# Kernel tuning notes

Hardware: AMD Instinct MI355X
Metric: run time of the kernel (lower is better)

Reference implementation:

```python
import jax, jax.numpy as jnp
import numpy as np
import math

HIDDEN = 2048
N_HEADS = 32
N_KV_HEADS = 8
HEAD_DIM = HIDDEN // N_HEADS
KV_REPEATS = N_HEADS // N_KV_HEADS
INTER = 4 * HIDDEN
EPS = 1e-5
B, Q, K = 2, 2048, 2048


def setup_inputs() -> dict:
    key = jax.random.key(0)
    ks = jax.random.split(key, 10)
    s = 0.02
    return {
        "hidden_states": jax.random.normal(ks[0], (B, Q, HIDDEN), jnp.float32),
        "key_states": jax.random.normal(ks[1], (B, K, N_KV_HEADS, HEAD_DIM), jnp.float32),
        "value_states": jax.random.normal(ks[2], (B, K, N_KV_HEADS, HEAD_DIM), jnp.float32),
        "gmu_memory": jnp.zeros((1,), jnp.float32),
        "w_ln1": jnp.ones((HIDDEN,), jnp.float32),
        "w_ln2": jnp.ones((HIDDEN,), jnp.float32),
        "w_q": jax.random.normal(ks[3], (N_HEADS * HEAD_DIM, HIDDEN), jnp.float32) * s,
        "w_o": jax.random.normal(ks[4], (HIDDEN, N_HEADS * HEAD_DIM), jnp.float32) * s,
        "w_gate": jax.random.normal(ks[5], (INTER, HIDDEN), jnp.float32) * s,
        "w_up": jax.random.normal(ks[6], (INTER, HIDDEN), jnp.float32) * s,
        "w_down": jax.random.normal(ks[7], (HIDDEN, INTER), jnp.float32) * s,
        "cu_seqlens_q": jnp.array([0, 1024, 2048], jnp.int32),
        "cu_seqlens_k": jnp.array([0, 1024, 2048], jnp.int32),
    }


def _rms_norm(x, w, eps=EPS):
    var = jnp.mean(jnp.square(x), axis=-1, keepdims=True)
    return (x * jax.lax.rsqrt(var + eps)) * w


def _segment_ids(cu, length):
    # position p belongs to segment i iff cu[i] <= p < cu[i+1]
    return jnp.searchsorted(cu[1:], jnp.arange(length), side="right")


def _attn_mask(q_len, k_len, cu_q, cu_k, causal=True, window_size=None):
    seg_q = _segment_ids(cu_q, q_len)  # [Q]
    seg_k = _segment_ids(cu_k, k_len)  # [K]
    mask = seg_q[:, None] == seg_k[None, :]
    if causal:
        q_pos = jnp.arange(q_len)[:, None]
        k_pos = jnp.arange(k_len)[None, :]
        offset = max(k_len - q_len, 0)
        mask = mask & (k_pos <= q_pos + offset)
    if window_size is not None and window_size > 0:
        q_pos = jnp.arange(q_len)[:, None] + max(k_len - q_len, 0)
        k_pos = jnp.arange(k_len)[None, :]
        mask = mask & (q_pos - k_pos < window_size)
    return mask  # [Q, K] bool


def reference(hidden_states, key_states, value_states, gmu_memory,
              w_ln1, w_ln2, w_q, w_o, w_gate, w_up, w_down,
              cu_seqlens_q, cu_seqlens_k):
    b, q_len, _ = hidden_states.shape
    residual = hidden_states
    normed = _rms_norm(hidden_states, w_ln1)

    # --- cross attention (shared KV, GQA) ---
    q = (normed @ w_q.T).reshape(b, q_len, N_HEADS, HEAD_DIM)
    k = jnp.repeat(key_states, KV_REPEATS, axis=2)    # [B,K,H,hd]
    v = jnp.repeat(value_states, KV_REPEATS, axis=2)  # [B,K,H,hd]
    k_len = k.shape[1]

    scores = jnp.einsum("bqhd,bkhd->bhqk", q, k) / math.sqrt(HEAD_DIM)
    mask = _attn_mask(q_len, k_len, cu_seqlens_q, cu_seqlens_k, causal=True)
    neg = jnp.finfo(scores.dtype).min
    scores = jnp.where(mask[None, None, :, :], scores, neg)
    probs = jax.nn.softmax(scores.astype(jnp.float32), axis=-1).astype(q.dtype)
    attn = jnp.einsum("bhqk,bkhd->bqhd", probs, v).reshape(b, q_len, -1)
    mixed = attn @ w_o.T

    hidden = residual + mixed

    # --- Llama MLP: down(silu(gate(x)) * up(x)) ---
    normed2 = _rms_norm(hidden, w_ln2)
    mlp = (jax.nn.silu(normed2 @ w_gate.T) * (normed2 @ w_up.T)) @ w_down.T
    return hidden + mlp
```

## Files before the change

### kernel.cpp

```cpp
#include <hip/hip_runtime.h>

typedef __bf16 bf16_t;
typedef bf16_t bf16x8 __attribute__((ext_vector_type(8)));
typedef float floatx4 __attribute__((ext_vector_type(4)));

#define HIDDEN 2048
#define NHEADS 32
#define NKV 8
#define HD 64
#define INTER 8192
#define SEQQ 2048
#define SEQK 2048
#define NBATCH 2
#define NEGBIG (-3.0e38f)

__device__ __forceinline__ floatx4 mfma16(bf16x8 a, bf16x8 b, floatx4 c) {
  return __builtin_amdgcn_mfma_f32_16x16x32_bf16(a, b, c, 0, 0, 0);
}

__device__ __forceinline__ uint4 pack8(const float* __restrict__ p) {
  float4 f0 = *(const float4*)p;
  float4 f1 = *(const float4*)(p + 4);
  union { uint4 u; bf16_t e[8]; } r;
  r.e[0] = (bf16_t)f0.x; r.e[1] = (bf16_t)f0.y; r.e[2] = (bf16_t)f0.z; r.e[3] = (bf16_t)f0.w;
  r.e[4] = (bf16_t)f1.x; r.e[5] = (bf16_t)f1.y; r.e[6] = (bf16_t)f1.z; r.e[7] = (bf16_t)f1.w;
  return r.u;
}

__global__ __launch_bounds__(256) void cvt_kernel(const float* __restrict__ src,
                                                  bf16_t* __restrict__ dst, int n8) {
  const int stride = gridDim.x * 256;
  for (int i = blockIdx.x * 256 + threadIdx.x; i < n8; i += stride)
    *(uint4*)(dst + (size_t)i * 8) = pack8(src + (size_t)i * 8);
}

__global__ __launch_bounds__(256) void rmsnorm_kernel(const float* __restrict__ x,
                                                      const float* __restrict__ w,
                                                      bf16_t* __restrict__ y) {
  const int row = blockIdx.x;
  const int tid = threadIdx.x;
  const float* xr = x + (size_t)row * HIDDEN + tid * 8;
  float4 x0 = *(const float4*)xr;
  float4 x1 = *(const float4*)(xr + 4);
  float xf[8] = {x0.x, x0.y, x0.z, x0.w, x1.x, x1.y, x1.z, x1.w};
  float ss = 0.f;
#pragma unroll
  for (int j = 0; j < 8; ++j) ss += xf[j] * xf[j];
#pragma unroll
  for (int off = 32; off >= 1; off >>= 1) ss += __shfl_xor(ss, off);
  __shared__ float red[4];
  if ((tid & 63) == 0) red[tid >> 6] = ss;
  __syncthreads();
  float tot = red[0] + red[1] + red[2] + red[3];
  float rs = 1.0f / sqrtf(tot / (float)HIDDEN + 1e-5f);
  const float* wr = w + tid * 8;
  float4 w0 = *(const float4*)wr;
  float4 w1 = *(const float4*)(wr + 4);
  float wf[8] = {w0.x, w0.y, w0.z, w0.w, w1.x, w1.y, w1.z, w1.w};
  bf16x8 ov;
#pragma unroll
  for (int j = 0; j < 8; ++j) ov[j] = (bf16_t)(xf[j] * rs * wf[j]);
  *(bf16x8*)(y + (size_t)row * HIDDEN + tid * 8) = ov;
}

template <int ROWS>
__device__ __forceinline__ void stage_tile(bf16_t* lds, const bf16_t* src, int ldK) {
  const int tid = (int)threadIdx.x;
  const int wid = tid >> 6;
  const int row0 = tid >> 3;
  const int scol = (((tid & 7) ^ (row0 & 7)) * 8);
#pragma unroll
  for (int i = 0; i < ROWS / 32; ++i) {
    const bf16_t* g = src + (size_t)(i * 32 + row0) * ldK + scol;
    __builtin_amdgcn_global_load_lds(
        (const __attribute__((address_space(1))) void*)g,
        (__attribute__((address_space(3))) void*)(lds + i * 2048 + wid * 512), 16, 0, 0);
  }
}

__device__ __forceinline__ bf16x8 ldfrag(const bf16_t* lds, int row, int kslot) {
  return *(const bf16x8*)(lds + row * 64 + ((kslot ^ (row & 7)) * 8));
}

template <int EPI, typename CT>
__global__ __launch_bounds__(256) void gemm_bt16(const bf16_t* __restrict__ A,
                                                 const bf16_t* __restrict__ W,
                                                 const float* __restrict__ resid,
                                                 CT* __restrict__ C, int Kd, int N) {
  const int m0 = blockIdx.y * 128, n0 = blockIdx.x * 128;
  const int tid = threadIdx.x;
  const int wid = tid >> 6, lane = tid & 63, quad = lane >> 4, l15 = lane & 15;
  const int wr = wid >> 1, wc = wid & 1;
  __shared__ __align__(16) bf16_t Asm[128 * 64];
  __shared__ __align__(16) bf16_t Bsm[128 * 64];
  floatx4 acc[4][4];
  floatx4 zero = {0.f, 0.f, 0.f, 0.f};
#pragma unroll
  for (int mi = 0; mi < 4; ++mi)
#pragma unroll
    for (int ni = 0; ni < 4; ++ni) acc[mi][ni] = zero;

  const bf16_t* Ab = A + (size_t)m0 * Kd;
  const bf16_t* Wb = W + (size_t)n0 * Kd;

  for (int kt = 0; kt < Kd; kt += 64) {
    __syncthreads();
    stage_tile<128>(Asm, Ab + kt, Kd);
    stage_tile<128>(Bsm, Wb + kt, Kd);
    __syncthreads();
#pragma unroll
    for (int kk = 0; kk < 2; ++kk) {
      const int ks = kk * 4 + quad;
      bf16x8 af[4], bfr[4];
#pragma unroll
      for (int mi = 0; mi < 4; ++mi) af[mi] = ldfrag(Asm, wr * 64 + mi * 16 + l15, ks);
#pragma unroll
      for (int ni = 0; ni < 4; ++ni) bfr[ni] = ldfrag(Bsm, wc * 64 + ni * 16 + l15, ks);
#pragma unroll
      for (int mi = 0; mi < 4; ++mi)
#pragma unroll
        for (int ni = 0; ni < 4; ++ni) acc[mi][ni] = mfma16(af[mi], bfr[ni], acc[mi][ni]);
    }
  }

#pragma unroll
  for (int mi = 0; mi < 4; ++mi) {
    const int mb = m0 + wr * 64 + mi * 16 + quad * 4;
#pragma unroll
    for (int ni = 0; ni < 4; ++ni) {
      const int n = n0 + wc * 64 + ni * 16 + l15;
      floatx4 v = acc[mi][ni];
#pragma unroll
      for (int r = 0; r < 4; ++r) {
        size_t idx = (size_t)(mb + r) * N + n;
        float val = v[r];
        if (EPI == 1) val += resid[idx];
        C[idx] = (CT)val;
      }
    }
  }
}

__global__ __launch_bounds__(256) void gateup16(const bf16_t* __restrict__ A,
                                                const bf16_t* __restrict__ Wg,
                                                const bf16_t* __restrict__ Wu,
                                                bf16_t* __restrict__ C, int Kd, int N) {
  const int m0 = blockIdx.y * 128, n0 = blockIdx.x * 64;
  const int tid = threadIdx.x;
  const int wid = tid >> 6, lane = tid & 63, quad = lane >> 4, l15 = lane & 15;
  const int wr = wid >> 1, wc = wid & 1;
  __shared__ __align__(16) bf16_t Asm[128 * 64];
  __shared__ __align__(16) bf16_t Gsm[64 * 64];
  __shared__ __align__(16) bf16_t Usm[64 * 64];
  floatx4 accg[4][2], accu[4][2];
  floatx4 zero = {0.f, 0.f, 0.f, 0.f};
#pragma unroll
  for (int mi = 0; mi < 4; ++mi)
#pragma unroll
    for (int ni = 0; ni < 2; ++ni) { accg[mi][ni] = zero; accu[mi][ni] = zero; }

  const bf16_t* Ab = A + (size_t)m0 * Kd;
  const bf16_t* Gb = Wg + (size_t)n0 * Kd;
  const bf16_t* Ub = Wu + (size_t)n0 * Kd;

  for (int kt = 0; kt < Kd; kt += 64) {
    __syncthreads();
    stage_tile<128>(Asm, Ab + kt, Kd);
    stage_tile<64>(Gsm, Gb + kt, Kd);
    stage_tile<64>(Usm, Ub + kt, Kd);
    __syncthreads();
#pragma unroll
    for (int kk = 0; kk < 2; ++kk) {
      const int ks = kk * 4 + quad;
      bf16x8 af[4];
#pragma unroll
      for (int mi = 0; mi < 4; ++mi) af[mi] = ldfrag(Asm, wr * 64 + mi * 16 + l15, ks);
#pragma unroll
      for (int ni = 0; ni < 2; ++ni) {
        bf16x8 bg = ldfrag(Gsm, wc * 32 + ni * 16 + l15, ks);
        bf16x8 bu = ldfrag(Usm, wc * 32 + ni * 16 + l15, ks);
#pragma unroll
        for (int mi = 0; mi < 4; ++mi) {
          accg[mi][ni] = mfma16(af[mi], bg, accg[mi][ni]);
          accu[mi][ni] = mfma16(af[mi], bu, accu[mi][ni]);
        }
      }
    }
  }

#pragma unroll
  for (int mi = 0; mi < 4; ++mi) {
    const int mb = m0 + wr * 64 + mi * 16 + quad * 4;
#pragma unroll
    for (int ni = 0; ni < 2; ++ni) {
      const int n = n0 + wc * 32 + ni * 16 + l15;
#pragma unroll
      for (int r = 0; r < 4; ++r) {
        float g = accg[mi][ni][r];
        float u = accu[mi][ni][r];
        float act = g / (1.f + __expf(-g)) * u;
        C[(size_t)(mb + r) * N + n] = (bf16_t)act;
      }
    }
  }
}

__global__ __launch_bounds__(256) void attn_gqa(const bf16_t* __restrict__ qbuf,
                                                const bf16_t* __restrict__ kbuf,
                                                const bf16_t* __restrict__ vbuf,
                                                const int* __restrict__ cuq,
                                                const int* __restrict__ cuk,
                                                bf16_t* __restrict__ obuf) {
  const int qt = blockIdx.x, hg = blockIdx.y, b = blockIdx.z;
  const int hk = hg >> 1;
  const int tid = threadIdx.x;
  const int wid = tid >> 6, lane = tid & 63, quad = lane >> 4, l15 = lane & 15;
  const int h = hg * 2 + (wid >> 1);
  const int qh = wid & 1;
  __shared__ __align__(16) bf16_t Vt[2][64 * 72];
  __shared__ __align__(16) bf16_t Pt[4 * 32 * 72];
  const int cq1 = cuq[1], ck1 = cuk[1];

  bf16x8 qf[2][2];
#pragma unroll
  for (int mi = 0; mi < 2; ++mi) {
    const int qr = qt * 64 + qh * 32 + mi * 16 + l15;
    const bf16_t* qp = qbuf + ((size_t)(b * SEQQ + qr)) * HIDDEN + h * HD;
    qf[mi][0] = *(const bf16x8*)(qp + quad * 8);
    qf[mi][1] = *(const bf16x8*)(qp + 32 + quad * 8);
  }

  floatx4 Of[2][4];
  floatx4 zero = {0.f, 0.f, 0.f, 0.f};
#pragma unroll
  for (int mi = 0; mi < 2; ++mi)
#pragma unroll
    for (int df = 0; df < 4; ++df) Of[mi][df] = zero;
  float m_r[2][4], l_r[2][4];
#pragma unroll
  for (int mi = 0; mi < 2; ++mi)
#pragma unroll
    for (int r = 0; r < 4; ++r) { m_r[mi][r] = -1e30f; l_r[mi][r] = 0.f; }

  const bool blk_seg1 = (qt * 64 >= cq1);
  const int kt_start = blk_seg1 ? (ck1 >> 6) : 0;

  const int vrow = tid >> 3;
  const int vc = (tid & 7) * 8;

#pragma unroll
  for (int i = 0; i < 2; ++i) {
    const int row = vrow + i * 32;
    const size_t goff = ((size_t)((b * SEQK + kt_start * 64 + row) * NKV + hk)) * HD + vc;
    bf16x8 vv = *(const bf16x8*)(vbuf + goff);
#pragma unroll
    for (int j = 0; j < 8; ++j) Vt[kt_start & 1][(vc + j) * 72 + row] = vv[j];
  }

  for (int kt = kt_start; kt <= qt; ++kt) {
    const int p = kt & 1;
    const bool hn = (kt < qt);
    bf16x8 vvn[2];
    if (hn) {
#pragma unroll
      for (int i = 0; i < 2; ++i) {
        const int row = vrow + i * 32;
        const size_t goff = ((size_t)((b * SEQK + (kt + 1) * 64 + row) * NKV + hk)) * HD + vc;
        vvn[i] = *(const bf16x8*)(vbuf + goff);
      }
    }
    bf16x8 kf[4][2];
#pragma unroll
    for (int nf = 0; nf < 4; ++nf) {
      const int krow = kt * 64 + nf * 16 + l15;
      const bf16_t* kp = kbuf + ((size_t)((b * SEQK + krow) * NKV + hk)) * HD;
      kf[nf][0] = *(const bf16x8*)(kp + quad * 8);
      kf[nf][1] = *(const bf16x8*)(kp + 32 + quad * 8);
    }
    floatx4 sf[2][4];
#pragma unroll
    for (int mi = 0; mi < 2; ++mi)
#pragma unroll
      for (int nf = 0; nf < 4; ++nf) {
        floatx4 a = zero;
        a = mfma16(qf[mi][0], kf[nf][0], a);
        a = mfma16(qf[mi][1], kf[nf][1], a);
        sf[mi][nf] = a;
      }

    float tmax[2][4];
#pragma unroll
    for (int mi = 0; mi < 2; ++mi) {
      const int q0 = qt * 64 + qh * 32 + mi * 16 + quad * 4;
#pragma unroll
      for (int r = 0; r < 4; ++r) tmax[mi][r] = NEGBIG;
#pragma unroll
      for (int nf = 0; nf < 4; ++nf) {
        const int kg = kt * 64 + nf * 16 + l15;
        const int sk = (kg >= ck1) ? 1 : 0;
#pragma unroll
        for (int r = 0; r < 4; ++r) {
          const int qg = q0 + r;
          const int sq = (qg >= cq1) ? 1 : 0;
          float s = sf[mi][nf][r] * 0.125f;
          bool ok = (kg <= qg) && (sk == sq);
          s = ok ? s : NEGBIG;
          sf[mi][nf][r] = s;
          tmax[mi][r] = fmaxf(tmax[mi][r], s);
        }
      }
#pragma unroll
      for (int r = 0; r < 4; ++r) {
#pragma unroll
        for (int off = 1; off <= 8; off <<= 1)
          tmax[mi][r] = fmaxf(tmax[mi][r], __shfl_xor(tmax[mi][r], off));
      }
    }
    float alpha[2][4], rsum[2][4];
#pragma unroll
    for (int mi = 0; mi < 2; ++mi)
#pragma unroll
      for (int r = 0; r < 4; ++r) {
        float mn = fmaxf(m_r[mi][r], tmax[mi][r]);
        alpha[mi][r] = __expf(m_r[mi][r] - mn);
        m_r[mi][r] = mn;
        rsum[mi][r] = 0.f;
      }
#pragma unroll
    for (int mi = 0; mi < 2; ++mi)
#pragma unroll
      for (int nf = 0; nf < 4; ++nf)
#pragma unroll
        for (int r = 0; r < 4; ++r) {
          float pv = __expf(sf[mi][nf][r] - m_r[mi][r]);
          rsum[mi][r] += pv;
          Pt[(wid * 32 + mi * 16 + quad * 4 + r) * 72 + nf * 16 + l15] = (bf16_t)pv;
        }
#pragma unroll
    for (int mi = 0; mi < 2; ++mi)
#pragma unroll
      for (int r = 0; r < 4; ++r) {
#pragma unroll
        for (int off = 1; off <= 8; off <<= 1) rsum[mi][r] += __shfl_xor(rsum[mi][r], off);
        l_r[mi][r] = alpha[mi][r] * l_r[mi][r] + rsum[mi][r];
      }
#pragma unroll
    for (int mi = 0; mi < 2; ++mi)
#pragma unroll
      for (int df = 0; df < 4; ++df)
#pragma unroll
        for (int r = 0; r < 4; ++r) Of[mi][df][r] *= alpha[mi][r];

    __syncthreads();

    if (hn) {
#pragma unroll
      for (int i = 0; i < 2; ++i) {
        const int row = vrow + i * 32;
#pragma unroll
        for (int j = 0; j < 8; ++j) Vt[p ^ 1][(vc + j) * 72 + row] = vvn[i][j];
      }
    }

#pragma unroll
    for (int kk = 0; kk < 2; ++kk) {
#pragma unroll
      for (int mi = 0; mi < 2; ++mi) {
        bf16x8 pfr = *(const bf16x8*)&Pt[(wid * 32 + mi * 16 + l15) * 72 + kk * 32 + quad * 8];
#pragma unroll
        for (int df = 0; df < 4; ++df) {
          bf16x8 vfr = *(const bf16x8*)&Vt[p][(df * 16 + l15) * 72 + kk * 32 + quad * 8];
          Of[mi][df] = mfma16(pfr, vfr, Of[mi][df]);
        }
      }
    }
  }

#pragma unroll
  for (int mi = 0; mi < 2; ++mi) {
    const int q0 = qt * 64 + qh * 32 + mi * 16 + quad * 4;
#pragma unroll
    for (int r = 0; r < 4; ++r) {
      float inv = (l_r[mi][r] > 0.f) ? 1.f / l_r[mi][r] : 0.f;
#pragma unroll
      for (int df = 0; df < 4; ++df) {
        obuf[((size_t)(b * SEQQ + q0 + r)) * HIDDEN + h * HD + df * 16 + l15] =
            (bf16_t)(Of[mi][df][r] * inv);
      }
    }
  }
}

template <int EPI, typename CT>
__global__ __launch_bounds__(256) void gemm_bt(const bf16_t* __restrict__ A,
                                               const float* __restrict__ W,
                                               const float* __restrict__ resid,
                                               CT* __restrict__ C,
                                               int Kd, int N) {
  const int m0 = blockIdx.y * 128, n0 = blockIdx.x * 128;
  const int tid = threadIdx.x;
  const int wid = tid >> 6, lane = tid & 63, quad = lane >> 4, l15 = lane & 15;
  const int wr = wid >> 1, wc = wid & 1;
  __shared__ __align__(16) bf16_t Asm[128 * 40];
  __shared__ __align__(16) bf16_t Bsm[128 * 40];
  floatx4 acc[4][4];
  floatx4 zero = {0.f, 0.f, 0.f, 0.f};
#pragma unroll
  for (int mi = 0; mi < 4; ++mi)
#pragma unroll
    for (int ni = 0; ni < 4; ++ni) acc[mi][ni] = zero;

  const int r0 = tid >> 2;
  const int c0 = (tid & 3) * 8;

  for (int kt = 0; kt < Kd; kt += 32) {
    __syncthreads();
    uint4 a0 = *(const uint4*)(A + (size_t)(m0 + r0) * Kd + kt + c0);
    uint4 a1 = *(const uint4*)(A + (size_t)(m0 + r0 + 64) * Kd + kt + c0);
    uint4 b0 = pack8(W + (size_t)(n0 + r0) * Kd + kt + c0);
    uint4 b1 = pack8(W + (size_t)(n0 + r0 + 64) * Kd + kt + c0);
    *(uint4*)&Asm[r0 * 40 + c0] = a0;
    *(uint4*)&Asm[(r0 + 64) * 40 + c0] = a1;
    *(uint4*)&Bsm[r0 * 40 + c0] = b0;
    *(uint4*)&Bsm[(r0 + 64) * 40 + c0] = b1;
    __syncthreads();
    bf16x8 af[4], bfrag[4];
#pragma unroll
    for (int mi = 0; mi < 4; ++mi)
      af[mi] = *(const bf16x8*)&Asm[(wr * 64 + mi * 16 + l15) * 40 + quad * 8];
#pragma unroll
    for (int ni = 0; ni < 4; ++ni)
      bfrag[ni] = *(const bf16x8*)&Bsm[(wc * 64 + ni * 16 + l15) * 40 + quad * 8];
#pragma unroll
    for (int mi = 0; mi < 4; ++mi)
#pragma unroll
      for (int ni = 0; ni < 4; ++ni)
        acc[mi][ni] = mfma16(af[mi], bfrag[ni], acc[mi][ni]);
  }

#pragma unroll
  for (int mi = 0; mi < 4; ++mi) {
    const int mb = m0 + wr * 64 + mi * 16 + quad * 4;
#pragma unroll
    for (int ni = 0; ni < 4; ++ni) {
      const int n = n0 + wc * 64 + ni * 16 + l15;
      floatx4 v = acc[mi][ni];
#pragma unroll
      for (int r = 0; r < 4; ++r) {
        size_t idx = (size_t)(mb + r) * N + n;
        float val = v[r];
        if (EPI == 1) val += resid[idx];
        C[idx] = (CT)val;
      }
    }
  }
}

__global__ __launch_bounds__(256) void gemm_gateup(const bf16_t* __restrict__ A,
                                                   const float* __restrict__ Wg,
                                                   const float* __restrict__ Wu,
                                                   bf16_t* __restrict__ C,
                                                   int Kd, int N) {
  const int m0 = blockIdx.y * 128, n0 = blockIdx.x * 128;
  const int tid = threadIdx.x;
  const int wid = tid >> 6, lane = tid & 63, quad = lane >> 4, l15 = lane & 15;
  const int wr = wid >> 1, wc = wid & 1;
  __shared__ __align__(16) bf16_t Asm[128 * 40];
  __shared__ __align__(16) bf16_t Gsm[128 * 40];
  __shared__ __align__(16) bf16_t Usm[128 * 40];
  floatx4 accg[4][4], accu[4][4];
  floatx4 zero = {0.f, 0.f, 0.f, 0.f};
#pragma unroll
  for (int mi = 0; mi < 4; ++mi)
#pragma unroll
    for (int ni = 0; ni < 4; ++ni) { accg[mi][ni] = zero; accu[mi][ni] = zero; }

  const int r0 = tid >> 2;
  const int c0 = (tid & 3) * 8;

  for (int kt = 0; kt < Kd; kt += 32) {
    __syncthreads();
    uint4 a0 = *(const uint4*)(A + (size_t)(m0 + r0) * Kd + kt + c0);
    uint4 a1 = *(const uint4*)(A + (size_t)(m0 + r0 + 64) * Kd + kt + c0);
    uint4 g0 = pack8(Wg + (size_t)(n0 + r0) * Kd + kt + c0);
    uint4 g1 = pack8(Wg + (size_t)(n0 + r0 + 64) * Kd + kt + c0);
    uint4 u0 = pack8(Wu + (size_t)(n0 + r0) * Kd + kt + c0);
    uint4 u1 = pack8(Wu + (size_t)(n0 + r0 + 64) * Kd + kt + c0);
    *(uint4*)&Asm[r0 * 40 + c0] = a0;
    *(uint4*)&Asm[(r0 + 64) * 40 + c0] = a1;
    *(uint4*)&Gsm[r0 * 40 + c0] = g0;
    *(uint4*)&Gsm[(r0 + 64) * 40 + c0] = g1;
    *(uint4*)&Usm[r0 * 40 + c0] = u0;
    *(uint4*)&Usm[(r0 + 64) * 40 + c0] = u1;
    __syncthreads();
    bf16x8 af[4];
#pragma unroll
    for (int mi = 0; mi < 4; ++mi)
      af[mi] = *(const bf16x8*)&Asm[(wr * 64 + mi * 16 + l15) * 40 + quad * 8];
#pragma unroll
    for (int ni = 0; ni < 4; ++ni) {
      bf16x8 bg = *(const bf16x8*)&Gsm[(wc * 64 + ni * 16 + l15) * 40 + quad * 8];
      bf16x8 bu = *(const bf16x8*)&Usm[(wc * 64 + ni * 16 + l15) * 40 + quad * 8];
#pragma unroll
      for (int mi = 0; mi < 4; ++mi) {
        accg[mi][ni] = mfma16(af[mi], bg, accg[mi][ni]);
        accu[mi][ni] = mfma16(af[mi], bu, accu[mi][ni]);
      }
    }
  }

#pragma unroll
  for (int mi = 0; mi < 4; ++mi) {
    const int mb = m0 + wr * 64 + mi * 16 + quad * 4;
#pragma unroll
    for (int ni = 0; ni < 4; ++ni) {
      const int n = n0 + wc * 64 + ni * 16 + l15;
#pragma unroll
      for (int r = 0; r < 4; ++r) {
        float g = accg[mi][ni][r];
        float u = accu[mi][ni][r];
        float act = g / (1.f + __expf(-g)) * u;
        C[(size_t)(mb + r) * N + n] = (bf16_t)act;
      }
    }
  }
}

__global__ __launch_bounds__(256) void attn_kernel(const bf16_t* __restrict__ qbuf,
                                                   const float* __restrict__ kbuf,
                                                   const float* __restrict__ vbuf,
                                                   const int* __restrict__ cuq,
                                                   const int* __restrict__ cuk,
                                                   bf16_t* __restrict__ obuf) {
  const int qt = blockIdx.x, h = blockIdx.y, b = blockIdx.z;
  const int hk = h >> 2;
  const int tid = threadIdx.x;
  const int wid = tid >> 6, lane = tid & 63, quad = lane >> 4, l15 = lane & 15;
  __shared__ __align__(16) bf16_t Kt[64 * 72];
  __shared__ __align__(16) bf16_t Vt[64 * 72];
  __shared__ __align__(16) bf16_t Pt[64 * 72];
  const int cq1 = cuq[1], ck1 = cuk[1];

  const int qrow_a = qt * 64 + wid * 16 + l15;
  const bf16_t* qp = qbuf + ((size_t)(b * SEQQ + qrow_a)) * HIDDEN + h * HD;
  bf16x8 qf0 = *(const bf16x8*)(qp + quad * 8);
  bf16x8 qf1 = *(const bf16x8*)(qp + 32 + quad * 8);

  floatx4 Of[4];
  floatx4 zero = {0.f, 0.f, 0.f, 0.f};
#pragma unroll
  for (int df = 0; df < 4; ++df) Of[df] = zero;
  float m_r[4], l_r[4];
#pragma unroll
  for (int r = 0; r < 4; ++r) { m_r[r] = -1e30f; l_r[r] = 0.f; }
  const int q_row0 = qt * 64 + wid * 16 + quad * 4;
  int seg_q[4];
#pragma unroll
  for (int r = 0; r < 4; ++r) seg_q[r] = (q_row0 + r >= cq1) ? 1 : 0;
  const bool blk_seg1 = (qt * 64 >= cq1);

  const int stag_row = tid >> 3;
  const int stag_c = (tid & 7) * 8;
  const int kt_start = blk_seg1 ? (ck1 >> 6) : 0;

  for (int kt = kt_start; kt <= qt; ++kt) {
    __syncthreads();
#pragma unroll
    for (int i = 0; i < 2; ++i) {
      const int row = stag_row + i * 32;
      const size_t goff = ((size_t)((b * SEQK + kt * 64 + row) * NKV + hk)) * HD + stag_c;
      uint4 kv = pack8(kbuf + goff);
      *(uint4*)&Kt[row * 72 + stag_c] = kv;
      union { uint4 u; bf16_t e[8]; } vv;
      vv.u = pack8(vbuf + goff);
#pragma unroll
      for (int j = 0; j < 8; ++j) Vt[(stag_c + j) * 72 + row] = vv.e[j];
    }
    __syncthreads();

    floatx4 sf[4];
#pragma unroll
    for (int nf = 0; nf < 4; ++nf) {
      bf16x8 kf0 = *(const bf16x8*)&Kt[(nf * 16 + l15) * 72 + quad * 8];
      bf16x8 kf1 = *(const bf16x8*)&Kt[(nf * 16 + l15) * 72 + 32 + quad * 8];
      floatx4 a = zero;
      a = mfma16(qf0, kf0, a);
      a = mfma16(qf1, kf1, a);
      sf[nf] = a;
    }

    float tmax[4];
#pragma unroll
    for (int r = 0; r < 4; ++r) tmax[r] = NEGBIG;
#pragma unroll
    for (int nf = 0; nf < 4; ++nf) {
      const int kg = kt * 64 + nf * 16 + l15;
#pragma unroll
      for (int r = 0; r < 4; ++r) {
        const int qg = q_row0 + r;
        const int sk = (kg >= ck1) ? 1 : 0;
        float s = sf[nf][r] * 0.125f;
        bool ok = (kg <= qg) && (sk == seg_q[r]);
        s = ok ? s : NEGBIG;
        sf[nf][r] = s;
        tmax[r] = fmaxf(tmax[r], s);
      }
    }
#pragma unroll
    for (int r = 0; r < 4; ++r) {
#pragma unroll
      for (int off = 1; off <= 8; off <<= 1) tmax[r] = fmaxf(tmax[r], __shfl_xor(tmax[r], off));
    }
    float alpha[4], rsum[4];
#pragma unroll
    for (int r = 0; r < 4; ++r) {
      float mn = fmaxf(m_r[r], tmax[r]);
      alpha[r] = __expf(m_r[r] - mn);
      m_r[r] = mn;
      rsum[r] = 0.f;
    }
#pragma unroll
    for (int nf = 0; nf < 4; ++nf) {
#pragma unroll
      for (int r = 0; r < 4; ++r) {
        float p = __expf(sf[nf][r] - m_r[r]);
        rsum[r] += p;
        Pt[(wid * 16 + quad * 4 + r) * 72 + nf * 16 + l15] = (bf16_t)p;
      }
    }
#pragma unroll
    for (int r = 0; r < 4; ++r) {
#pragma unroll
      for (int off = 1; off <= 8; off <<= 1) rsum[r] += __shfl_xor(rsum[r], off);
      l_r[r] = alpha[r] * l_r[r] + rsum[r];
    }
#pragma unroll
    for (int df = 0; df < 4; ++df) {
#pragma unroll
      for (int r = 0; r < 4; ++r) Of[df][r] *= alpha[r];
    }
#pragma unroll
    for (int kk = 0; kk < 2; ++kk) {
      bf16x8 pf = *(const bf16x8*)&Pt[(wid * 16 + l15) * 72 + kk * 32 + quad * 8];
#pragma unroll
      for (int df = 0; df < 4; ++df) {
        bf16x8 vf = *(const bf16x8*)&Vt[(df * 16 + l15) * 72 + kk * 32 + quad * 8];
        Of[df] = mfma16(pf, vf, Of[df]);
      }
    }
  }

  float inv[4];
#pragma unroll
  for (int r = 0; r < 4; ++r) inv[r] = (l_r[r] > 0.f) ? 1.f / l_r[r] : 0.f;
#pragma unroll
  for (int df = 0; df < 4; ++df) {
#pragma unroll
    for (int r = 0; r < 4; ++r) {
      obuf[((size_t)(b * SEQQ + q_row0 + r)) * HIDDEN + h * HD + df * 16 + l15] =
          (bf16_t)(Of[df][r] * inv[r]);
    }
  }
}

static inline int cvt_grid(int n8) {
  int g = (n8 + 255) / 256;
  return g > 2048 ? 2048 : g;
}

extern "C" void kernel_launch(void* const* d_in, const int* in_sizes, int n_in,
                              void* d_out, int out_size, void* d_ws, size_t ws_size,
                              hipStream_t stream) {
  const float* x    = (const float*)d_in[0];
  const float* kst  = (const float*)d_in[1];
  const float* vst  = (const float*)d_in[2];
  const float* wln1 = (const float*)d_in[4];
  const float* wln2 = (const float*)d_in[5];
  const float* wq   = (const float*)d_in[6];
  const float* wo   = (const float*)d_in[7];
  const float* wg   = (const float*)d_in[8];
  const float* wu   = (const float*)d_in[9];
  const float* wd   = (const float*)d_in[10];
  const int* cuq    = (const int*)d_in[11];
  const int* cuk    = (const int*)d_in[12];
  float* out = (float*)d_out;

  const size_t MB = 1024ull * 1024ull;
  char* ws = (char*)d_ws;
  const bool full = ws_size >= 200 * MB;
  const bool conv = ws_size >= 168 * MB;

  if (conv) {
    bf16_t* bufA = (bf16_t*)ws;
    bf16_t* bufB = (bf16_t*)(ws + 16 * MB);
    char* p = ws + 16 * MB + (full ? 64 : 32) * MB;
    bf16_t* wq16 = (bf16_t*)p; p += 8 * MB;
    bf16_t* wo16 = (bf16_t*)p; p += 8 * MB;
    bf16_t* wg16 = (bf16_t*)p; p += 32 * MB;
    bf16_t* wu16 = (bf16_t*)p; p += 32 * MB;
    bf16_t* wd16 = (bf16_t*)p; p += 32 * MB;
    bf16_t* k16  = (bf16_t*)p; p += 4 * MB;
    bf16_t* v16  = (bf16_t*)p;

    const int n8_qo = 2048 * 2048 / 8;
    const int n8_gud = 8192 * 2048 / 8;
    const int n8_kv = NBATCH * SEQK * NKV * HD / 8;
    cvt_kernel<<<cvt_grid(n8_qo), 256, 0, stream>>>(wq, wq16, n8_qo);
    cvt_kernel<<<cvt_grid(n8_qo), 256, 0, stream>>>(wo, wo16, n8_qo);
    cvt_kernel<<<cvt_grid(n8_gud), 256, 0, stream>>>(wg, wg16, n8_gud);
    cvt_kernel<<<cvt_grid(n8_gud), 256, 0, stream>>>(wu, wu16, n8_gud);
    cvt_kernel<<<cvt_grid(n8_gud), 256, 0, stream>>>(wd, wd16, n8_gud);
    cvt_kernel<<<cvt_grid(n8_kv), 256, 0, stream>>>(kst, k16, n8_kv);
    cvt_kernel<<<cvt_grid(n8_kv), 256, 0, stream>>>(vst, v16, n8_kv);

    rmsnorm_kernel<<<4096, 256, 0, stream>>>(x, wln1, bufA);
    gemm_bt16<0, bf16_t><<<dim3(16, 32), 256, 0, stream>>>(bufA, wq16, nullptr, bufB, 2048, 2048);
    attn_gqa<<<dim3(32, 16, 2), 256, 0, stream>>>(bufB, k16, v16, cuq, cuk, bufA);
    gemm_bt16<1, float><<<dim3(16, 32), 256, 0, stream>>>(bufA, wo16, x, out, 2048, 2048);
    rmsnorm_kernel<<<4096, 256, 0, stream>>>(out, wln2, bufA);
    const int nch = full ? 1 : 2;
    const int mch = 4096 / nch;
    for (int c = 0; c < nch; ++c) {
      const size_t off = (size_t)c * mch;
      gateup16<<<dim3(128, mch / 128), 256, 0, stream>>>(bufA + off * HIDDEN, wg16, wu16,
                                                         bufB, 2048, 8192);
      gemm_bt16<1, float><<<dim3(16, mch / 128), 256, 0, stream>>>(bufB, wd16, out + off * HIDDEN,
                                                                   out + off * HIDDEN, 8192, 2048);
    }
  } else {
    bf16_t* bufA = (bf16_t*)ws;
    bf16_t* bufB = (bf16_t*)(ws + 16 * MB);
    rmsnorm_kernel<<<4096, 256, 0, stream>>>(x, wln1, bufA);
    gemm_bt<0, bf16_t><<<dim3(16, 32), 256, 0, stream>>>(bufA, wq, nullptr, bufB, 2048, 2048);
    attn_kernel<<<dim3(32, 32, 2), 256, 0, stream>>>(bufB, kst, vst, cuq, cuk, bufA);
    gemm_bt<1, float><<<dim3(16, 32), 256, 0, stream>>>(bufA, wo, x, out, 2048, 2048);
    rmsnorm_kernel<<<4096, 256, 0, stream>>>(out, wln2, bufA);
    for (int c = 0; c < 2; ++c) {
      const size_t off = (size_t)c * 2048;
      gemm_gateup<<<dim3(64, 16), 256, 0, stream>>>(bufA + off * HIDDEN, wg, wu, bufB, 2048, 8192);
      gemm_bt<1, float><<<dim3(16, 16), 256, 0, stream>>>(bufB, wd, out + off * HIDDEN,
                                                          out + off * HIDDEN, 8192, 2048);
    }
  }
}
```

Before: 1.012 ms.

## Fuse weight conversions, remap GEMM blocks across XCDs, streamline attention softmax

New measurement: 1.086 ms. 7.2% more time.

```diff
diff --git a/kernel.cpp b/kernel.cpp
--- a/kernel.cpp
+++ b/kernel.cpp
@@ -13,6 +13,7 @@
 #define SEQK 2048
 #define NBATCH 2
 #define NEGBIG (-3.0e38f)
+#define CE 0.18033688011112042f
 
 __device__ __forceinline__ floatx4 mfma16(bf16x8 a, bf16x8 b, floatx4 c) {
   return __builtin_amdgcn_mfma_f32_16x16x32_bf16(a, b, c, 0, 0, 0);
@@ -27,11 +28,29 @@
   return r.u;
 }
 
-__global__ __launch_bounds__(256) void cvt_kernel(const float* __restrict__ src,
-                                                  bf16_t* __restrict__ dst, int n8) {
-  const int stride = gridDim.x * 256;
-  for (int i = blockIdx.x * 256 + threadIdx.x; i < n8; i += stride)
-    *(uint4*)(dst + (size_t)i * 8) = pack8(src + (size_t)i * 8);
+struct Cvt7 {
+  const float *s0, *s1, *s2, *s3, *s4, *s5, *s6;
+  bf16_t *d0, *d1, *d2, *d3, *d4, *d5, *d6;
+  int n0, n1, n2, n3, n4, n5, n6;
+  int c1, c2, c3, c4, c5, c6, c7;
+};
+
+__global__ __launch_bounds__(256) void cvt7_kernel(Cvt7 a) {
+  const int bid = blockIdx.x;
+  const float* s; bf16_t* d; int n8; int b0;
+  if      (bid < a.c1) { s = a.s0; d = a.d0; n8 = a.n0; b0 = 0; }
+  else if (bid < a.c2) { s = a.s1; d = a.d1; n8 = a.n1; b0 = a.c1; }
+  else if (bid < a.c3) { s = a.s2; d = a.d2; n8 = a.n2; b0 = a.c2; }
+  else if (bid < a.c4) { s = a.s3; d = a.d3; n8 = a.n3; b0 = a.c3; }
+  else if (bid < a.c5) { s = a.s4; d = a.d4; n8 = a.n4; b0 = a.c4; }
+  else if (bid < a.c6) { s = a.s5; d = a.d5; n8 = a.n5; b0 = a.c5; }
+  else                 { s = a.s6; d = a.d6; n8 = a.n6; b0 = a.c6; }
+  const int base = (bid - b0) * 1024 + threadIdx.x;
+#pragma unroll
+  for (int it = 0; it < 4; ++it) {
+    const int i = base + it * 256;
+    if (i < n8) *(uint4*)(d + (size_t)i * 8) = pack8(s + (size_t)i * 8);
+  }
 }
 
 __global__ __launch_bounds__(256) void rmsnorm_kernel(const float* __restrict__ x,
@@ -82,12 +101,27 @@
   return *(const bf16x8*)(lds + row * 64 + ((kslot ^ (row & 7)) * 8));
 }
 
+__device__ __forceinline__ void xcd_map(int nbx, int nby, int* bx, int* by) {
+  const int nwg = nbx * nby;
+  const int L = (int)blockIdx.y * nbx + (int)blockIdx.x;
+  if ((nwg & 7) == 0) {
+    const int t = (L & 7) * (nwg >> 3) + (L >> 3);
+    *bx = t / nby;
+    *by = t - *bx * nby;
+  } else {
+    *bx = (int)blockIdx.x;
+    *by = (int)blockIdx.y;
+  }
+}
+
 template <int EPI, typename CT>
 __global__ __launch_bounds__(256) void gemm_bt16(const bf16_t* __restrict__ A,
                                                  const bf16_t* __restrict__ W,
                                                  const float* __restrict__ resid,
                                                  CT* __restrict__ C, int Kd, int N) {
-  const int m0 = blockIdx.y * 128, n0 = blockIdx.x * 128;
+  int bx, by;
+  xcd_map(gridDim.x, gridDim.y, &bx, &by);
+  const int m0 = by * 128, n0 = bx * 128;
   const int tid = threadIdx.x;
   const int wid = tid >> 6, lane = tid & 63, quad = lane >> 4, l15 = lane & 15;
   const int wr = wid >> 1, wc = wid & 1;
@@ -145,7 +179,9 @@
                                                 const bf16_t* __restrict__ Wg,
                                                 const bf16_t* __restrict__ Wu,
                                                 bf16_t* __restrict__ C, int Kd, int N) {
-  const int m0 = blockIdx.y * 128, n0 = blockIdx.x * 64;
+  int bx, by;
+  xcd_map(gridDim.x, gridDim.y, &bx, &by);
+  const int m0 = by * 128, n0 = bx * 64;
   const int tid = threadIdx.x;
   const int wid = tid >> 6, lane = tid & 63, quad = lane >> 4, l15 = lane & 15;
   const int wr = wid >> 1, wc = wid & 1;
@@ -220,6 +256,7 @@
   __shared__ __align__(16) bf16_t Vt[2][64 * 72];
   __shared__ __align__(16) bf16_t Pt[4 * 32 * 72];
   const int cq1 = cuq[1], ck1 = cuk[1];
+  const bool aligned = (cq1 == ck1) && ((ck1 & 63) == 0);
 
   bf16x8 qf[2][2];
 #pragma unroll
@@ -269,61 +306,72 @@
         vvn[i] = *(const bf16x8*)(vbuf + goff);
       }
     }
-    bf16x8 kf[4][2];
+    floatx4 sf[2][4];
 #pragma unroll
     for (int nf = 0; nf < 4; ++nf) {
       const int krow = kt * 64 + nf * 16 + l15;
       const bf16_t* kp = kbuf + ((size_t)((b * SEQK + krow) * NKV + hk)) * HD;
-      kf[nf][0] = *(const bf16x8*)(kp + quad * 8);
-      kf[nf][1] = *(const bf16x8*)(kp + 32 + quad * 8);
-    }
-    floatx4 sf[2][4];
+      bf16x8 kf0 = *(const bf16x8*)(kp + quad * 8);
+      bf16x8 kf1 = *(const bf16x8*)(kp + 32 + quad * 8);
+#pragma unroll
+      for (int mi = 0; mi < 2; ++mi) {
+        floatx4 a = zero;
+        a = mfma16(qf[mi][0], kf0, a);
+        a = mfma16(qf[mi][1], kf1, a);
+        sf[mi][nf] = a;
+      }
+    }
+
+    float tmax[2][4];
+    const bool need_mask = (kt == qt) || !aligned;
+    if (need_mask) {
+#pragma unroll
+      for (int mi = 0; mi < 2; ++mi) {
+        const int q0 = qt * 64 + qh * 32 + mi * 16 + quad * 4;
+#pragma unroll
+        for (int r = 0; r < 4; ++r) tmax[mi][r] = NEGBIG;
+#pragma unroll
+        for (int nf = 0; nf < 4; ++nf) {
+          const int kg = kt * 64 + nf * 16 + l15;
+          const int sk = (kg >= ck1) ? 1 : 0;
+#pragma unroll
+          for (int r = 0; r < 4; ++r) {
+            const int qg = q0 + r;
+            const int sq = (qg >= cq1) ? 1 : 0;
+            float s = sf[mi][nf][r];
+            bool ok = (kg <= qg) && (sk == sq);
+            s = ok ? s : NEGBIG;
+            sf[mi][nf][r] = s;
+            tmax[mi][r] = fmaxf(tmax[mi][r], s);
+          }
+        }
+      }
+    } else {
+#pragma unroll
+      for (int mi = 0; mi < 2; ++mi)
+#pragma unroll
+        for (int r = 0; r < 4; ++r)
+          tmax[mi][r] = fmaxf(fmaxf(sf[mi][0][r], sf[mi][1][r]),
+                              fmaxf(sf[mi][2][r], sf[mi][3][r]));
+    }
 #pragma unroll
     for (int mi = 0; mi < 2; ++mi)
-#pragma unroll
-      for (int nf = 0; nf < 4; ++nf) {
-        floatx4 a = zero;
-        a = mfma16(qf[mi][0], kf[nf][0], a);
-        a = mfma16(qf[mi][1], kf[nf][1], a);
-        sf[mi][nf] = a;
-      }
-
-    float tmax[2][4];
-#pragma unroll
-    for (int mi = 0; mi < 2; ++mi) {
-      const int q0 = qt * 64 + qh * 32 + mi * 16 + quad * 4;
-#pragma unroll
-      for (int r = 0; r < 4; ++r) tmax[mi][r] = NEGBIG;
-#pragma unroll
-      for (int nf = 0; nf < 4; ++nf) {
-        const int kg = kt * 64 + nf * 16 + l15;
-        const int sk = (kg >= ck1) ? 1 : 0;
-#pragma unroll
-        for (int r = 0; r < 4; ++r) {
-          const int qg = q0 + r;
-          const int sq = (qg >= cq1) ? 1 : 0;
-          float s = sf[mi][nf][r] * 0.125f;
-          bool ok = (kg <= qg) && (sk == sq);
-          s = ok ? s : NEGBIG;
-          sf[mi][nf][r] = s;
-          tmax[mi][r] = fmaxf(tmax[mi][r], s);
-        }
-      }
 #pragma unroll
       for (int r = 0; r < 4; ++r) {
 #pragma unroll
         for (int off = 1; off <= 8; off <<= 1)
           tmax[mi][r] = fmaxf(tmax[mi][r], __shfl_xor(tmax[mi][r], off));
       }
-    }
-    float alpha[2][4], rsum[2][4];
+
+    float alpha[2][4], rsum[2][4], mc[2][4];
 #pragma unroll
     for (int mi = 0; mi < 2; ++mi)
 #pragma unroll
       for (int r = 0; r < 4; ++r) {
         float mn = fmaxf(m_r[mi][r], tmax[mi][r]);
-        alpha[mi][r] = __expf(m_r[mi][r] - mn);
+        alpha[mi][r] = exp2f((m_r[mi][r] - mn) * CE);
         m_r[mi][r] = mn;
+        mc[mi][r] = mn * CE;
         rsum[mi][r] = 0.f;
       }
 #pragma unroll
@@ -332,7 +380,7 @@
       for (int nf = 0; nf < 4; ++nf)
 #pragma unroll
         for (int r = 0; r < 4; ++r) {
-          float pv = __expf(sf[mi][nf][r] - m_r[mi][r]);
+          float pv = exp2f(sf[mi][nf][r] * CE - mc[mi][r]);
           rsum[mi][r] += pv;
           Pt[(wid * 32 + mi * 16 + quad * 4 + r) * 72 + nf * 16 + l15] = (bf16_t)pv;
         }
@@ -661,11 +709,6 @@
           (bf16_t)(Of[df][r] * inv[r]);
     }
   }
-}
-
-static inline int cvt_grid(int n8) {
-  int g = (n8 + 255) / 256;
-  return g > 2048 ? 2048 : g;
 }
 
 extern "C" void kernel_launch(void* const* d_in, const int* in_sizes, int n_in,
@@ -705,13 +748,19 @@
     const int n8_qo = 2048 * 2048 / 8;
     const int n8_gud = 8192 * 2048 / 8;
     const int n8_kv = NBATCH * SEQK * NKV * HD / 8;
-    cvt_kernel<<<cvt_grid(n8_qo), 256, 0, stream>>>(wq, wq16, n8_qo);
-    cvt_kernel<<<cvt_grid(n8_qo), 256, 0, stream>>>(wo, wo16, n8_qo);
-    cvt_kernel<<<cvt_grid(n8_gud), 256, 0, stream>>>(wg, wg16, n8_gud);
-    cvt_kernel<<<cvt_grid(n8_gud), 256, 0, stream>>>(wu, wu16, n8_gud);
-    cvt_kernel<<<cvt_grid(n8_gud), 256, 0, stream>>>(wd, wd16, n8_gud);
-    cvt_kernel<<<cvt_grid(n8_kv), 256, 0, stream>>>(kst, k16, n8_kv);
-    cvt_kernel<<<cvt_grid(n8_kv), 256, 0, stream>>>(vst, v16, n8_kv);
+    Cvt7 a;
+    a.s0 = wq;  a.d0 = wq16; a.n0 = n8_qo;
+    a.s1 = wo;  a.d1 = wo16; a.n1 = n8_qo;
+    a.s2 = wg;  a.d2 = wg16; a.n2 = n8_gud;
+    a.s3 = wu;  a.d3 = wu16; a.n3 = n8_gud;
+    a.s4 = wd;  a.d4 = wd16; a.n4 = n8_gud;
+    a.s5 = kst; a.d5 = k16;  a.n5 = n8_kv;
+    a.s6 = vst; a.d6 = v16;  a.n6 = n8_kv;
+    const int bq = (n8_qo + 1023) / 1024, bg = (n8_gud + 1023) / 1024,
+              bk = (n8_kv + 1023) / 1024;
+    a.c1 = bq; a.c2 = bq * 2; a.c3 = bq * 2 + bg; a.c4 = bq * 2 + bg * 2;
+    a.c5 = bq * 2 + bg * 3; a.c6 = a.c5 + bk; a.c7 = a.c6 + bk;
+    cvt7_kernel<<<a.c7, 256, 0, stream>>>(a);
 
     rmsnorm_kernel<<<4096, 256, 0, stream>>>(x, wln1, bufA);
     gemm_bt16<0, bf16_t><<<dim3(16, 32), 256, 0, stream>>>(bufA, wq16, nullptr, bufB, 2048, 2048);
```
